# Optimization experiments

Measured on AMD Instinct MI355X. Metric: run time of the kernel, lower is better.

## Reference

```python
import jax, jax.numpy as jnp
import numpy as np

B, R, N, M, K = 4, 4, 4096, 64, 3
F_NUM = 512
KN = K * N


def _block(x, Ws, bs):
    """SO-Net PointResNet: 1x1 convs + ReLU; last layer sees concat(input, hidden)."""
    h = x
    for W, b in zip(Ws[:-1], bs[:-1]):
        h = jax.nn.relu(jnp.einsum('oc,bcn->bon', W, h) + b[None, :, None])
    h = jnp.concatenate([x, h], axis=1)
    return jax.nn.relu(jnp.einsum('oc,bcn->bon', Ws[-1], h) + bs[-1][None, :, None])


def _forward(x, intensity, node, node_knn_I, fpW, fpB, gpW, gpB):
    # --- som.query_topk: k nearest SOM nodes per point ---
    xd = jax.lax.stop_gradient(x)
    dist = jnp.sum((xd[:, :, :, None] - node[:, :, None, :]) ** 2, axis=1)      # B,N,M
    _, topk = jax.lax.top_k(-dist, K)                                           # B,N,K
    min_idx = topk.transpose(0, 2, 1).reshape(B, KN)                            # B,KN (k copies stacked)
    mask = jax.nn.one_hot(min_idx, M, dtype=jnp.float32)                        # B,KN,M
    mask_row_max = jnp.max(mask, axis=1) > 0                                    # B,M  node has >=1 point
    mask_row_sum = jnp.sum(mask, axis=1)                                        # B,M  points per node

    x_stack = jnp.tile(x, (1, 1, K))                                            # B,2,KN
    cluster_mean = jnp.einsum('bcn,bnm->bcm', jax.lax.stop_gradient(x_stack), mask) \
                   / (mask_row_sum[:, None, :] + 1e-5)                          # B,2,M (detached)

    # --- rotation group (2x2 rotations at angles 2*pi*r/R) ---
    theta = 2.0 * jnp.pi * jnp.arange(R, dtype=jnp.float32) / R
    c, s = jnp.cos(theta), jnp.sin(theta)
    rot = jnp.stack([jnp.stack([c, -s], -1), jnp.stack([s, c], -1)], -2)        # R,2,2

    x_rot = jnp.einsum('rij,bjn->brin', rot, x_stack)                           # B,R,2,KN
    node_rot = jnp.einsum('rij,bjm->brim', rot, cluster_mean)                   # B,R,2,M
    centers = jnp.take_along_axis(node_rot, min_idx[:, None, None, :], axis=3)  # B,R,2,KN
    x_dec = jax.lax.stop_gradient(x_rot - centers).reshape(B * R, 2, KN)

    # --- first PointResNet over all B*R rotation copies ---
    feat = _block(x_dec, fpW, fpB)                                              # BR,128,KN

    # --- index_max scatter-max per SOM cluster (value of argmax == segment max) ---
    seg = jnp.tile(min_idx[:, None, :], (1, R, 1)).reshape(B * R, KN)
    segmax = jax.vmap(lambda f, sgi: jax.ops.segment_max(f.T, sgi, num_segments=M).T)(feat, seg)
    rowmax = jnp.tile(mask_row_max[:, None, :], (1, R, 1)).reshape(B * R, M)
    pooled = jnp.where(rowmax[:, None, :], segmax, feat[:, :, 0:1])             # BR,128,M (empty -> gather idx 0)

    # --- final PointResNet over SOM nodes, then max over nodes and rotations ---
    g_in = jnp.concatenate([node_rot.reshape(B * R, 2, M), pooled], axis=1)     # BR,130,M
    out = _block(g_in, gpW, gpB)                                                # BR,F,M
    return out.reshape(B, R, F_NUM, M).max(axis=3).max(axis=1)                  # B,F


def setup_inputs() -> dict:
    key = jax.random.key(0)
    ks = jax.random.split(key, 24)
    d = {}
    d['x'] = jax.random.normal(ks[0], (B, 2, N), jnp.float32)
    d['intensity'] = jax.random.uniform(ks[1], (B, 1, N), jnp.float32)
    d['node'] = jax.random.normal(ks[2], (B, 2, M), jnp.float32)
    d['node_knn_I'] = jax.random.randint(ks[3], (B, M, 1), 0, M)
    dims_fp = [(64, 2), (64, 64), (128, 64), (128, 130)]      # PointResNet(2,[64,64,128,128])
    dims_gp = [(256, 130), (256, 256), (512, 256), (F_NUM, 642)]  # PointResNet(130,[256,256,512,F])
    i = 4
    for name, dims in (('fp', dims_fp), ('gp', dims_gp)):
        for j, (o, ci) in enumerate(dims):
            d[f'{name}_W{j}'] = jax.random.normal(ks[i], (o, ci), jnp.float32) / np.sqrt(ci).astype(np.float32)
            d[f'{name}_b{j}'] = jnp.zeros((o,), jnp.float32)
            i += 1
    return d


def reference(x, intensity, node, node_knn_I,
              fp_W0, fp_b0, fp_W1, fp_b1, fp_W2, fp_b2, fp_W3, fp_b3,
              gp_W0, gp_b0, gp_W1, gp_b1, gp_W2, gp_b2, gp_W3, gp_b3):
    return _forward(x, intensity, node, node_knn_I,
                    [fp_W0, fp_W1, fp_W2, fp_W3], [fp_b0, fp_b1, fp_b2, fp_b3],
                    [gp_W0, gp_W1, gp_W2, gp_W3], [gp_b0, gp_b1, gp_b2, gp_b3])
```

## Files before the change

### kernel.cpp

```cpp
#include <hip/hip_runtime.h>
#include <stdint.h>

#define BB 4
#define RR 4
#define NN 4096
#define MM 64
#define KK 3
#define KNN 12288
#define BRR 16
#define FF 512

typedef short bf16x8 __attribute__((ext_vector_type(8)));
typedef float f32x4 __attribute__((ext_vector_type(4)));

__device__ __forceinline__ float bf2f(unsigned int u) {
  union { unsigned int i; float f; } v; v.i = u << 16; return v.f;
}
__device__ __forceinline__ unsigned short f2bf(float f) {
  union { float f; unsigned int i; } v; v.f = f;
  unsigned int x = v.i;
  return (unsigned short)((x + 0x7fffu + ((x >> 16) & 1u)) >> 16);
}
__device__ __forceinline__ float ldf(const void* p, long i, int isbf) {
  if (isbf) return bf2f(((const unsigned short*)p)[i]);
  return ((const float*)p)[i];
}

__global__ __launch_bounds__(256) void k_detect(
    const unsigned short* __restrict__ x, int* __restrict__ flag) {
  __shared__ int bad;
  if (threadIdx.x == 0) bad = 0;
  __syncthreads();
  int cnt = 0;
  for (int i = threadIdx.x; i < 1024; i += 256) {
    unsigned short u = x[i * 2];
    int e = (u >> 7) & 0xFF;
    if (e >= 0x90 || (e > 0 && e <= 0x50)) ++cnt;
  }
  atomicAdd(&bad, cnt);
  __syncthreads();
  if (threadIdx.x == 0) flag[0] = (bad < 100) ? 1 : 0;
}

struct WPtrs { const void* p[7]; };
__global__ __launch_bounds__(256) void k_cvt(
    WPtrs wp, const int* __restrict__ flag, unsigned short* __restrict__ Wb) {
  const int e0=4096, e1=12288, e2=28928, e3=62208, e4=127744, e5=258816, e6=587520;
  int t = blockIdx.x * 256 + threadIdx.x;
  if (t >= e6) return;
  int s, base;
  if      (t < e0) { s=0; base=0;  }
  else if (t < e1) { s=1; base=e0; }
  else if (t < e2) { s=2; base=e1; }
  else if (t < e3) { s=3; base=e2; }
  else if (t < e4) { s=4; base=e3; }
  else if (t < e5) { s=5; base=e4; }
  else             { s=6; base=e5; }
  int local = t - base;
  unsigned short u;
  if (flag[0]) u = ((const unsigned short*)wp.p[s])[local];
  else         u = f2bf(((const float*)wp.p[s])[local]);
  Wb[t] = u;
}

__global__ __launch_bounds__(256) void k_assign(
    const void* __restrict__ x, const void* __restrict__ node,
    const int* __restrict__ flag, int* __restrict__ idx, float* __restrict__ csum,
    int* __restrict__ blkcnt) {
  __shared__ float nd[2][64];
  __shared__ float cs[192];
  int isbf = flag[0];
  int tid = threadIdx.x;
  int b = blockIdx.x >> 4;
  int n = ((blockIdx.x & 15) << 8) + tid;
  if (tid < 128) nd[tid >> 6][tid & 63] = ldf(node, b * 128 + tid, isbf);
  if (tid < 192) cs[tid] = 0.f;
  __syncthreads();
  float x0 = ldf(x, b * 8192 + n, isbf);
  float x1 = ldf(x, b * 8192 + 4096 + n, isbf);
  float d0 = 1e30f, d1 = 1e30f, d2 = 1e30f;
  int m0 = 0, m1 = 0, m2 = 0;
#pragma unroll 8
  for (int m = 0; m < 64; ++m) {
    float dx = x0 - nd[0][m];
    float dy = x1 - nd[1][m];
    float d = __fmul_rn(dx, dx) + __fmul_rn(dy, dy);
    if (d < d0)      { d2=d1; m2=m1; d1=d0; m1=m0; d0=d; m0=m; }
    else if (d < d1) { d2=d1; m2=m1; d1=d;  m1=m; }
    else if (d < d2) { d2=d;  m2=m; }
  }
  long base = ((long)b * NN + n) * 3;
  idx[base] = m0; idx[base + 1] = m1; idx[base + 2] = m2;
  atomicAdd(&cs[m0*3+0], x0); atomicAdd(&cs[m0*3+1], x1); atomicAdd(&cs[m0*3+2], 1.f);
  atomicAdd(&cs[m1*3+0], x0); atomicAdd(&cs[m1*3+1], x1); atomicAdd(&cs[m1*3+2], 1.f);
  atomicAdd(&cs[m2*3+0], x0); atomicAdd(&cs[m2*3+1], x1); atomicAdd(&cs[m2*3+2], 1.f);
  __syncthreads();
  if (tid < 192) atomicAdd(&csum[b * 192 + tid], cs[tid]);
  if (tid < 64) blkcnt[blockIdx.x * 64 + tid] = (int)cs[tid*3 + 2];
}

__global__ __launch_bounds__(256) void k_means(
    const float* __restrict__ csum, const int* __restrict__ blkcnt,
    float* __restrict__ noderot, int* __restrict__ rowflag,
    int* __restrict__ off, int* __restrict__ blkoff) {
  int t = threadIdx.x;
  int b = t >> 6, m = t & 63;
  float s0 = csum[b*192 + m*3], s1 = csum[b*192 + m*3 + 1], c = csum[b*192 + m*3 + 2];
  float mx = s0 / (c + 1e-5f);
  float my = s1 / (c + 1e-5f);
  rowflag[b * 64 + m] = (c > 0.f) ? 1 : 0;
  for (int r = 0; r < 4; ++r) {
    float th = 1.5707964f * (float)r;
    float cr = cosf(th), sr = sinf(th);
    noderot[((b*4 + r)*2 + 0)*64 + m] = cr*mx - sr*my;
    noderot[((b*4 + r)*2 + 1)*64 + m] = sr*mx + cr*my;
  }
  if (m == 0) {
    int acc = 0;
    for (int mm = 0; mm < 64; ++mm) {
      off[b*64 + mm] = acc;
      acc += (int)csum[b*192 + mm*3 + 2];
    }
  }
  __syncthreads();
  int base = off[b*64 + m];
  for (int blk = 0; blk < 16; ++blk) {
    blkoff[(b*16 + blk)*64 + m] = base;
    base += blkcnt[(b*16 + blk)*64 + m];
  }
}

__global__ __launch_bounds__(256) void k_scatter(
    const int* __restrict__ idx, const int* __restrict__ blkoff,
    int* __restrict__ sorted) {
  __shared__ int lc[64];
  int tid = threadIdx.x;
  int blk = blockIdx.x;
  int b = blk >> 4;
  int n = ((blk & 15) << 8) + tid;
  if (tid < 64) lc[tid] = 0;
  __syncthreads();
#pragma unroll
  for (int kk = 0; kk < 3; ++kk) {
    int m = idx[((long)b * NN + n) * 3 + kk];
    int pos = atomicAdd(&lc[m], 1);
    sorted[b * KNN + blkoff[blk*64 + m] + pos] = (m << 12) | n;
  }
}

__global__ __launch_bounds__(256) void k_fused(
    const void* __restrict__ x, const int* __restrict__ sorted,
    const int* __restrict__ idx, const float* __restrict__ noderot,
    const int* __restrict__ flag,
    const void* __restrict__ fW0, const void* __restrict__ fb0,
    const unsigned short* __restrict__ Wb,
    const void* __restrict__ fb1, const void* __restrict__ fb2,
    const void* __restrict__ fb3,
    unsigned int* __restrict__ pooled, float* __restrict__ feat0) {
  __shared__ unsigned short Cs[64 * 136];
  __shared__ unsigned short Hs[64 * 72];
  __shared__ int mcol[64];
  const unsigned short* fW1 = Wb;
  const unsigned short* fW2 = Wb + 4096;
  const unsigned short* fW3 = Wb + 12288;
  int isbf = flag[0];
  int tid = threadIdx.x, lane = tid & 63, wv = tid >> 6;
  int quad = lane >> 4, lr = lane & 15;
  int br = blockIdx.y, b = br >> 2, r = br & 3;
  if (tid < 64) {
    int e = sorted[b * KNN + blockIdx.x * 64 + tid];
    int m = e >> 12, n = e & 4095;
    int isz = (n == 0 && m == idx[(long)b * NN * 3]) ? 256 : 0;
    mcol[tid] = m | isz;
    float x0 = ldf(x, b*8192 + n, isbf), x1 = ldf(x, b*8192 + 4096 + n, isbf);
    float th = 1.5707964f * (float)r;
    float cr = cosf(th), sr = sinf(th);
    float xd0 = (cr*x0 - sr*x1) - noderot[(br*2 + 0)*64 + m];
    float xd1 = (sr*x0 + cr*x1) - noderot[(br*2 + 1)*64 + m];
    *(unsigned int*)&Cs[tid * 136] = (unsigned int)f2bf(xd0) | ((unsigned int)f2bf(xd1) << 16);
  }
  __syncthreads();
  {
    int col = tid & 63, og = (tid >> 6) << 4;
    unsigned int xu = *(unsigned int*)&Cs[col * 136];
    float fx0 = bf2f(xu & 0xffff), fx1 = bf2f(xu >> 16);
    union { bf16x8 v; unsigned short s[8]; } o8[2];
#pragma unroll
    for (int j = 0; j < 16; ++j) {
      int o = og + j;
      float h = ldf(fb0, o, isbf) + ldf(fW0, o*2, isbf) * fx0 + ldf(fW0, o*2+1, isbf) * fx1;
      o8[j >> 3].s[j & 7] = f2bf(fmaxf(h, 0.f));
    }
    *(bf16x8*)&Hs[col*72 + og]     = o8[0].v;
    *(bf16x8*)&Hs[col*72 + og + 8] = o8[1].v;
  }
  __syncthreads();
  {
    int o0 = wv * 16;
    f32x4 acc[4];
    float bb4[4];
#pragma unroll
    for (int rr = 0; rr < 4; ++rr) bb4[rr] = ldf(fb1, o0 + quad*4 + rr, isbf);
#pragma unroll
    for (int nt = 0; nt < 4; ++nt) acc[nt] = (f32x4){bb4[0], bb4[1], bb4[2], bb4[3]};
#pragma unroll
    for (int ks = 0; ks < 64; ks += 32) {
      bf16x8 a = *(const bf16x8*)(fW1 + (o0 + lr)*64 + ks + quad*8);
#pragma unroll
      for (int nt = 0; nt < 4; ++nt) {
        bf16x8 bf = *(bf16x8*)&Hs[(nt*16 + lr)*72 + ks + quad*8];
        acc[nt] = __builtin_amdgcn_mfma_f32_16x16x32_bf16(a, bf, acc[nt], 0, 0, 0);
      }
    }
    __syncthreads();
#pragma unroll
    for (int nt = 0; nt < 4; ++nt) {
      int col = nt*16 + lr;
      union { unsigned long long u; unsigned short s[4]; } pk;
#pragma unroll
      for (int rr = 0; rr < 4; ++rr) pk.s[rr] = f2bf(fmaxf(acc[nt][rr], 0.f));
      *(unsigned long long*)&Hs[col*72 + o0 + quad*4] = pk.u;
    }
  }
  __syncthreads();
#pragma unroll
  for (int p2 = 0; p2 < 2; ++p2) {
    int o0 = p2*64 + wv*16;
    f32x4 acc[4];
    float bb4[4];
#pragma unroll
    for (int rr = 0; rr < 4; ++rr) bb4[rr] = ldf(fb2, o0 + quad*4 + rr, isbf);
#pragma unroll
    for (int nt = 0; nt < 4; ++nt) acc[nt] = (f32x4){bb4[0], bb4[1], bb4[2], bb4[3]};
#pragma unroll
    for (int ks = 0; ks < 64; ks += 32) {
      bf16x8 a = *(const bf16x8*)(fW2 + (o0 + lr)*64 + ks + quad*8);
#pragma unroll
      for (int nt = 0; nt < 4; ++nt) {
        bf16x8 bf = *(bf16x8*)&Hs[(nt*16 + lr)*72 + ks + quad*8];
        acc[nt] = __builtin_amdgcn_mfma_f32_16x16x32_bf16(a, bf, acc[nt], 0, 0, 0);
      }
    }
#pragma unroll
    for (int nt = 0; nt < 4; ++nt) {
      int col = nt*16 + lr;
      int o = o0 + quad*4;
      unsigned int w0 = (unsigned int)f2bf(fmaxf(acc[nt][0], 0.f)) |
                        ((unsigned int)f2bf(fmaxf(acc[nt][1], 0.f)) << 16);
      unsigned int w1 = (unsigned int)f2bf(fmaxf(acc[nt][2], 0.f)) |
                        ((unsigned int)f2bf(fmaxf(acc[nt][3], 0.f)) << 16);
      *(unsigned int*)&Cs[col*136 + 2 + o] = w0;
      *(unsigned int*)&Cs[col*136 + 4 + o] = w1;
    }
  }
  __syncthreads();
  f32x4 acc3[2][4];
#pragma unroll
  for (int p3 = 0; p3 < 2; ++p3) {
    int o0 = p3*64 + wv*16;
    float bb4[4];
#pragma unroll
    for (int rr = 0; rr < 4; ++rr) bb4[rr] = ldf(fb3, o0 + quad*4 + rr, isbf);
#pragma unroll
    for (int nt = 0; nt < 4; ++nt) acc3[p3][nt] = (f32x4){bb4[0], bb4[1], bb4[2], bb4[3]};
#pragma unroll
    for (int ks = 0; ks < 128; ks += 32) {
      union { bf16x8 v; unsigned int u[4]; } au;
      const unsigned int* ap = (const unsigned int*)(fW3 + (long)(o0 + lr)*130 + ks + quad*8);
      au.u[0] = ap[0]; au.u[1] = ap[1]; au.u[2] = ap[2]; au.u[3] = ap[3];
#pragma unroll
      for (int nt = 0; nt < 4; ++nt) {
        bf16x8 bf = *(bf16x8*)&Cs[(nt*16 + lr)*136 + ks + quad*8];
        acc3[p3][nt] = __builtin_amdgcn_mfma_f32_16x16x32_bf16(au.v, bf, acc3[p3][nt], 0, 0, 0);
      }
    }
#pragma unroll
    for (int rr = 0; rr < 4; ++rr) {
      int o = o0 + quad*4 + rr;
      unsigned int wu = *(const unsigned int*)(fW3 + (long)o*130 + 128);
      float w0 = bf2f(wu & 0xffff), w1 = bf2f(wu >> 16);
#pragma unroll
      for (int nt = 0; nt < 4; ++nt) {
        unsigned int bu = *(unsigned int*)&Cs[(nt*16 + lr)*136 + 128];
        acc3[p3][nt][rr] += w0 * bf2f(bu & 0xffff) + w1 * bf2f(bu >> 16);
      }
    }
  }
  __syncthreads();
#pragma unroll
  for (int p3 = 0; p3 < 2; ++p3) {
    int o0 = p3*64 + wv*16;
#pragma unroll
    for (int nt = 0; nt < 4; ++nt) {
      int col = nt*16 + lr;
      union { unsigned long long u; unsigned short s[4]; } pk;
#pragma unroll
      for (int rr = 0; rr < 4; ++rr) pk.s[rr] = f2bf(fmaxf(acc3[p3][nt][rr], 0.f));
      *(unsigned long long*)&Cs[col*136 + o0 + quad*4] = pk.u;
    }
  }
  __syncthreads();
  {
    int o = tid & 127, h = tid >> 7;
    int c0 = h * 32;
    int curm = mcol[c0] & 255;
    float v = 0.f;
    for (int c = c0; c < c0 + 32; ++c) {
      int mc = mcol[c];
      int mm = mc & 255;
      float f = bf2f(Cs[c*136 + o]);
      if (mm != curm) {
        atomicMax(&pooled[(((long)br*64 + curm) << 7) + o], __float_as_uint(v));
        curm = mm; v = 0.f;
      }
      v = fmaxf(v, f);
      if (mc & 256) feat0[br*128 + o] = f;
    }
    atomicMax(&pooled[(((long)br*64 + curm) << 7) + o], __float_as_uint(v));
  }
}

__global__ __launch_bounds__(256) void k_finalize(
    const unsigned int* __restrict__ pooled, const float* __restrict__ feat0,
    const int* __restrict__ rowflag, const float* __restrict__ noderot,
    unsigned short* __restrict__ AG) {
  int t = blockIdx.x * 256 + threadIdx.x;
  int col = t >> 7, o = t & 127;
  int br = col >> 6, m = col & 63, b = br >> 2;
  float v = __uint_as_float(pooled[((long)col << 7) + o]);
  if (!rowflag[b*64 + m]) v = feat0[br*128 + o];
  AG[(long)col*648 + 2 + o] = f2bf(v);
  if (o < 2) AG[(long)col*648 + o] = f2bf(noderot[(br*2 + o)*64 + m]);
}

template<int KW, int KMAIN, bool REM2, int BSTR, int OSTR, int OOFF, int EPI>
__global__ __launch_bounds__(256) void k_gemm(
    const unsigned short* __restrict__ W, const void* __restrict__ bias,
    const int* __restrict__ flag,
    const unsigned short* __restrict__ Bb, unsigned short* __restrict__ Out,
    unsigned int* __restrict__ outmax) {
  int isbf = flag[0];
  int lane = threadIdx.x & 63;
  int wv = threadIdx.x >> 6;
  int quad = lane >> 4, lr = lane & 15;
  int o0 = blockIdx.y * 64 + wv * 16;
  long p0 = (long)blockIdx.x * 64;
  float bia[4];
#pragma unroll
  for (int rr = 0; rr < 4; ++rr) bia[rr] = ldf(bias, o0 + quad*4 + rr, isbf);
  f32x4 acc[4];
#pragma unroll
  for (int nt = 0; nt < 4; ++nt) acc[nt] = (f32x4){bia[0], bia[1], bia[2], bia[3]};
  const unsigned short* arow = W + (long)(o0 + lr) * KW;
  for (int ks = 0; ks < KMAIN; ks += 32) {
    bf16x8 a;
    if constexpr ((KW % 8) == 0) {
      a = *(const bf16x8*)(arow + ks + quad*8);
    } else {
      union { bf16x8 v; unsigned int u[4]; } au;
      const unsigned int* ap = (const unsigned int*)(arow + ks + quad*8);
      au.u[0] = ap[0]; au.u[1] = ap[1]; au.u[2] = ap[2]; au.u[3] = ap[3];
      a = au.v;
    }
#pragma unroll
    for (int nt = 0; nt < 4; ++nt) {
      bf16x8 bf = *(const bf16x8*)(Bb + (p0 + nt*16 + lr) * BSTR + ks + quad*8);
      acc[nt] = __builtin_amdgcn_mfma_f32_16x16x32_bf16(a, bf, acc[nt], 0, 0, 0);
    }
  }
  if constexpr (REM2) {
#pragma unroll
    for (int rr = 0; rr < 4; ++rr) {
      int o = o0 + quad*4 + rr;
      unsigned int wu = *(const unsigned int*)(W + (long)o * KW + KMAIN);
      float w0 = bf2f(wu & 0xffff), w1 = bf2f(wu >> 16);
#pragma unroll
      for (int nt = 0; nt < 4; ++nt) {
        long p = p0 + nt*16 + lr;
        unsigned int bu = *(const unsigned int*)(Bb + p * BSTR + KMAIN);
        acc[nt][rr] += w0 * bf2f(bu & 0xffff) + w1 * bf2f(bu >> 16);
      }
    }
  }
  if constexpr (EPI == 0) {
#pragma unroll
    for (int nt = 0; nt < 4; ++nt) {
      long p = p0 + nt*16 + lr;
      unsigned short v0 = f2bf(fmaxf(acc[nt][0], 0.f));
      unsigned short v1 = f2bf(fmaxf(acc[nt][1], 0.f));
      unsigned short v2 = f2bf(fmaxf(acc[nt][2], 0.f));
      unsigned short v3 = f2bf(fmaxf(acc[nt][3], 0.f));
      unsigned short* op = Out + p * OSTR + OOFF + o0 + quad*4;
      if constexpr (((OOFF * 2) % 8) == 0) {
        union { unsigned long long u; unsigned short s[4]; } pk;
        pk.s[0] = v0; pk.s[1] = v1; pk.s[2] = v2; pk.s[3] = v3;
        *(unsigned long long*)op = pk.u;
      } else {
        *(unsigned int*)op       = (unsigned int)v0 | ((unsigned int)v1 << 16);
        *(unsigned int*)(op + 2) = (unsigned int)v2 | ((unsigned int)v3 << 16);
      }
    }
  } else {
#pragma unroll
    for (int rr = 0; rr < 4; ++rr) {
      float v = fmaxf(fmaxf(acc[0][rr], acc[1][rr]), fmaxf(acc[2][rr], acc[3][rr]));
      v = fmaxf(v, 0.f);
      v = fmaxf(v, __shfl_xor(v, 1, 64));
      v = fmaxf(v, __shfl_xor(v, 2, 64));
      v = fmaxf(v, __shfl_xor(v, 4, 64));
      v = fmaxf(v, __shfl_xor(v, 8, 64));
      if (lr == 0) {
        int bb2 = (int)(blockIdx.x >> 2);
        atomicMax(&outmax[bb2 * FF + o0 + quad*4 + rr], __float_as_uint(v));
      }
    }
  }
}

__global__ __launch_bounds__(256) void k_out(
    const unsigned int* __restrict__ outmax, const int* __restrict__ flag,
    void* __restrict__ out) {
  int t = blockIdx.x * 256 + threadIdx.x;
  float v = __uint_as_float(outmax[t]);
  if (flag[0]) ((unsigned short*)out)[t] = f2bf(v);
  else         ((float*)out)[t] = v;
}

extern "C" void kernel_launch(void* const* d_in, const int* in_sizes, int n_in,
                              void* d_out, int out_size, void* d_ws, size_t ws_size,
                              hipStream_t stream) {
  const void* x    = d_in[0];
  const void* node = d_in[2];
  const void* fpW0 = d_in[4];  const void* fpb0 = d_in[5];
  const void* fpW1 = d_in[6];  const void* fpb1 = d_in[7];
  const void* fpW2 = d_in[8];  const void* fpb2 = d_in[9];
  const void* fpW3 = d_in[10]; const void* fpb3 = d_in[11];
  const void* gpW0 = d_in[12]; const void* gpb0 = d_in[13];
  const void* gpW1 = d_in[14]; const void* gpb1 = d_in[15];
  const void* gpW2 = d_in[16]; const void* gpb2 = d_in[17];
  const void* gpW3 = d_in[18]; const void* gpb3 = d_in[19];

  char* ws = (char*)d_ws;
  int*            flag    = (int*)(ws + 0);
  float*          csum    = (float*)(ws + 256);
  unsigned int*   outmax  = (unsigned int*)(ws + 3328);
  unsigned int*   pooled  = (unsigned int*)(ws + 11520);
  int*            idx     = (int*)(ws + 535808);
  int*            blkcnt  = (int*)(ws + 732416);
  int*            blkoff  = (int*)(ws + 748800);
  int*            off     = (int*)(ws + 765184);
  float*          noderot = (float*)(ws + 766208);
  int*            rowflag = (int*)(ws + 774400);
  int*            sorted  = (int*)(ws + 775424);
  float*          feat0   = (float*)(ws + 972032);
  unsigned short* AG      = (unsigned short*)(ws + 980224);
  unsigned short* Hg1     = (unsigned short*)(ws + 2307328);
  unsigned short* Hg2     = (unsigned short*)(ws + 2831616);
  unsigned short* Wb      = (unsigned short*)(ws + 3355904);

  hipMemsetAsync(ws, 0, 535808, stream);

  k_detect<<<1, 256, 0, stream>>>((const unsigned short*)x, flag);
  WPtrs wp; wp.p[0]=fpW1; wp.p[1]=fpW2; wp.p[2]=fpW3; wp.p[3]=gpW0;
  wp.p[4]=gpW1; wp.p[5]=gpW2; wp.p[6]=gpW3;
  k_cvt<<<2295, 256, 0, stream>>>(wp, flag, Wb);

  k_assign<<<64, 256, 0, stream>>>(x, node, flag, idx, csum, blkcnt);
  k_means<<<1, 256, 0, stream>>>(csum, blkcnt, noderot, rowflag, off, blkoff);
  k_scatter<<<64, 256, 0, stream>>>(idx, blkoff, sorted);
  k_fused<<<dim3(192, 16), 256, 0, stream>>>(x, sorted, idx, noderot, flag,
                                             fpW0, fpb0, Wb, fpb1, fpb2, fpb3,
                                             pooled, feat0);
  k_finalize<<<512, 256, 0, stream>>>(pooled, feat0, rowflag, noderot, AG);

  const unsigned short* gW0 = Wb + 28928;
  const unsigned short* gW1 = Wb + 62208;
  const unsigned short* gW2 = Wb + 127744;
  const unsigned short* gW3 = Wb + 258816;
  k_gemm<130, 128, true, 648, 256, 0, 0><<<dim3(16, 4), 256, 0, stream>>>(gW0, gpb0, flag, AG, Hg1, nullptr);
  k_gemm<256, 256, false, 256, 256, 0, 0><<<dim3(16, 4), 256, 0, stream>>>(gW1, gpb1, flag, Hg1, Hg2, nullptr);
  k_gemm<256, 256, false, 256, 648, 130, 0><<<dim3(16, 8), 256, 0, stream>>>(gW2, gpb2, flag, Hg2, AG, nullptr);
  k_gemm<642, 640, true, 648, 0, 0, 2><<<dim3(16, 8), 256, 0, stream>>>(gW3, gpb3, flag, AG, nullptr, outmax);

  k_out<<<8, 256, 0, stream>>>(outmax, flag, d_out);
}
```

Baseline: 199.2 us.

## Fuse front-end kernels, swizzle LDS tiles, use packed bf16 convert instruction

Merges the dtype detection, weight conversion and SOM assignment into one launch, and folds the means/prefix-offset kernel into the scatter kernel, cutting five small launches to two. Every block now redoes the small detection scan, and each scatter block recomputes prefix sums serially. LDS row offsets for the Hs and Cs tiles get an XOR swizzle to reduce bank conflicts on the MFMA operand reads. Scalar bf16 rounding is replaced with the v_cvt_pk_bf16_f32 instruction everywhere, which may round differently at the edges.

Measured after the change: 199.4 us. Within noise of the previous version (+0.1%).

```diff
diff --git a/kernel.cpp b/kernel.cpp
--- a/kernel.cpp
+++ b/kernel.cpp
@@ -21,58 +21,66 @@
   unsigned int x = v.i;
   return (unsigned short)((x + 0x7fffu + ((x >> 16) & 1u)) >> 16);
 }
+__device__ __forceinline__ unsigned int cvtpk(float a, float b) {
+  unsigned int r;
+  asm("v_cvt_pk_bf16_f32 %0, %1, %2" : "=v"(r) : "v"(a), "v"(b));
+  return r;
+}
 __device__ __forceinline__ float ldf(const void* p, long i, int isbf) {
   if (isbf) return bf2f(((const unsigned short*)p)[i]);
   return ((const float*)p)[i];
 }
-
-__global__ __launch_bounds__(256) void k_detect(
-    const unsigned short* __restrict__ x, int* __restrict__ flag) {
+__device__ __forceinline__ int hsw(int col, int so) { return col * 72  + (so ^ (col & 24)); }
+__device__ __forceinline__ int csw(int col, int so) { return col * 136 + (so ^ (col & 24)); }
+
+struct WPtrs { const void* p[7]; };
+
+__global__ __launch_bounds__(256) void k_front(
+    const void* __restrict__ x, const void* __restrict__ node, WPtrs wp,
+    int* __restrict__ flag, unsigned short* __restrict__ Wb,
+    int* __restrict__ idx, float* __restrict__ csum, int* __restrict__ blkcnt) {
   __shared__ int bad;
-  if (threadIdx.x == 0) bad = 0;
-  __syncthreads();
-  int cnt = 0;
-  for (int i = threadIdx.x; i < 1024; i += 256) {
-    unsigned short u = x[i * 2];
-    int e = (u >> 7) & 0xFF;
-    if (e >= 0x90 || (e > 0 && e <= 0x50)) ++cnt;
-  }
-  atomicAdd(&bad, cnt);
-  __syncthreads();
-  if (threadIdx.x == 0) flag[0] = (bad < 100) ? 1 : 0;
-}
-
-struct WPtrs { const void* p[7]; };
-__global__ __launch_bounds__(256) void k_cvt(
-    WPtrs wp, const int* __restrict__ flag, unsigned short* __restrict__ Wb) {
-  const int e0=4096, e1=12288, e2=28928, e3=62208, e4=127744, e5=258816, e6=587520;
-  int t = blockIdx.x * 256 + threadIdx.x;
-  if (t >= e6) return;
-  int s, base;
-  if      (t < e0) { s=0; base=0;  }
-  else if (t < e1) { s=1; base=e0; }
-  else if (t < e2) { s=2; base=e1; }
-  else if (t < e3) { s=3; base=e2; }
-  else if (t < e4) { s=4; base=e3; }
-  else if (t < e5) { s=5; base=e4; }
-  else             { s=6; base=e5; }
-  int local = t - base;
-  unsigned short u;
-  if (flag[0]) u = ((const unsigned short*)wp.p[s])[local];
-  else         u = f2bf(((const float*)wp.p[s])[local]);
-  Wb[t] = u;
-}
-
-__global__ __launch_bounds__(256) void k_assign(
-    const void* __restrict__ x, const void* __restrict__ node,
-    const int* __restrict__ flag, int* __restrict__ idx, float* __restrict__ csum,
-    int* __restrict__ blkcnt) {
   __shared__ float nd[2][64];
   __shared__ float cs[192];
-  int isbf = flag[0];
   int tid = threadIdx.x;
-  int b = blockIdx.x >> 4;
-  int n = ((blockIdx.x & 15) << 8) + tid;
+  if (tid == 0) bad = 0;
+  __syncthreads();
+  {
+    const unsigned short* xs = (const unsigned short*)x;
+    int cnt = 0;
+    for (int i = tid; i < 1024; i += 256) {
+      unsigned short u = xs[i * 2];
+      int e = (u >> 7) & 0xFF;
+      if (e >= 0x90 || (e > 0 && e <= 0x50)) ++cnt;
+    }
+    atomicAdd(&bad, cnt);
+  }
+  __syncthreads();
+  int isbf = (bad < 100) ? 1 : 0;
+  if (blockIdx.x == 0 && tid == 0) flag[0] = isbf;
+
+  if (blockIdx.x < 2295) {
+    const int e0=4096, e1=12288, e2=28928, e3=62208, e4=127744, e5=258816, e6=587520;
+    int t = blockIdx.x * 256 + tid;
+    if (t >= e6) return;
+    int s, base;
+    if      (t < e0) { s=0; base=0;  }
+    else if (t < e1) { s=1; base=e0; }
+    else if (t < e2) { s=2; base=e1; }
+    else if (t < e3) { s=3; base=e2; }
+    else if (t < e4) { s=4; base=e3; }
+    else if (t < e5) { s=5; base=e4; }
+    else             { s=6; base=e5; }
+    int local = t - base;
+    unsigned short u;
+    if (isbf) u = ((const unsigned short*)wp.p[s])[local];
+    else      u = f2bf(((const float*)wp.p[s])[local]);
+    Wb[t] = u;
+    return;
+  }
+  int bi = blockIdx.x - 2295;
+  int b = bi >> 4;
+  int n = ((bi & 15) << 8) + tid;
   if (tid < 128) nd[tid >> 6][tid & 63] = ldf(node, b * 128 + tid, isbf);
   if (tid < 192) cs[tid] = 0.f;
   __syncthreads();
@@ -96,55 +104,47 @@
   atomicAdd(&cs[m2*3+0], x0); atomicAdd(&cs[m2*3+1], x1); atomicAdd(&cs[m2*3+2], 1.f);
   __syncthreads();
   if (tid < 192) atomicAdd(&csum[b * 192 + tid], cs[tid]);
-  if (tid < 64) blkcnt[blockIdx.x * 64 + tid] = (int)cs[tid*3 + 2];
-}
-
-__global__ __launch_bounds__(256) void k_means(
+  if (tid < 64) blkcnt[bi * 64 + tid] = (int)cs[tid*3 + 2];
+}
+
+__global__ __launch_bounds__(256) void k_scatter2(
     const float* __restrict__ csum, const int* __restrict__ blkcnt,
-    float* __restrict__ noderot, int* __restrict__ rowflag,
-    int* __restrict__ off, int* __restrict__ blkoff) {
-  int t = threadIdx.x;
-  int b = t >> 6, m = t & 63;
-  float s0 = csum[b*192 + m*3], s1 = csum[b*192 + m*3 + 1], c = csum[b*192 + m*3 + 2];
-  float mx = s0 / (c + 1e-5f);
-  float my = s1 / (c + 1e-5f);
-  rowflag[b * 64 + m] = (c > 0.f) ? 1 : 0;
-  for (int r = 0; r < 4; ++r) {
-    float th = 1.5707964f * (float)r;
-    float cr = cosf(th), sr = sinf(th);
-    noderot[((b*4 + r)*2 + 0)*64 + m] = cr*mx - sr*my;
-    noderot[((b*4 + r)*2 + 1)*64 + m] = sr*mx + cr*my;
-  }
-  if (m == 0) {
-    int acc = 0;
-    for (int mm = 0; mm < 64; ++mm) {
-      off[b*64 + mm] = acc;
-      acc += (int)csum[b*192 + mm*3 + 2];
-    }
-  }
-  __syncthreads();
-  int base = off[b*64 + m];
-  for (int blk = 0; blk < 16; ++blk) {
-    blkoff[(b*16 + blk)*64 + m] = base;
-    base += blkcnt[(b*16 + blk)*64 + m];
-  }
-}
-
-__global__ __launch_bounds__(256) void k_scatter(
-    const int* __restrict__ idx, const int* __restrict__ blkoff,
-    int* __restrict__ sorted) {
+    const int* __restrict__ idx, int* __restrict__ sorted,
+    float* __restrict__ noderot, int* __restrict__ rowflag) {
+  __shared__ int scnt[64];
+  __shared__ int soff[64];
   __shared__ int lc[64];
   int tid = threadIdx.x;
   int blk = blockIdx.x;
-  int b = blk >> 4;
+  int b = blk >> 4, chunk = blk & 15;
+  if (tid < 64) scnt[tid] = (int)csum[b*192 + tid*3 + 2];
+  __syncthreads();
+  if (tid < 64) {
+    int m = tid, acc = 0;
+    for (int mm = 0; mm < m; ++mm) acc += scnt[mm];
+    for (int c = 0; c < chunk; ++c) acc += blkcnt[(b*16 + c)*64 + m];
+    soff[m] = acc;
+    lc[m] = 0;
+    if (chunk == 0) {
+      float s0 = csum[b*192 + m*3], s1 = csum[b*192 + m*3 + 1], cc = csum[b*192 + m*3 + 2];
+      float mx = s0 / (cc + 1e-5f);
+      float my = s1 / (cc + 1e-5f);
+      rowflag[b*64 + m] = (cc > 0.f) ? 1 : 0;
+      for (int r = 0; r < 4; ++r) {
+        float th = 1.5707964f * (float)r;
+        float cr = cosf(th), sr = sinf(th);
+        noderot[((b*4 + r)*2 + 0)*64 + m] = cr*mx - sr*my;
+        noderot[((b*4 + r)*2 + 1)*64 + m] = sr*mx + cr*my;
+      }
+    }
+  }
+  __syncthreads();
   int n = ((blk & 15) << 8) + tid;
-  if (tid < 64) lc[tid] = 0;
-  __syncthreads();
 #pragma unroll
   for (int kk = 0; kk < 3; ++kk) {
     int m = idx[((long)b * NN + n) * 3 + kk];
     int pos = atomicAdd(&lc[m], 1);
-    sorted[b * KNN + blkoff[blk*64 + m] + pos] = (m << 12) | n;
+    sorted[b * KNN + soff[m] + pos] = (m << 12) | n;
   }
 }
 
@@ -177,22 +177,25 @@
     float cr = cosf(th), sr = sinf(th);
     float xd0 = (cr*x0 - sr*x1) - noderot[(br*2 + 0)*64 + m];
     float xd1 = (sr*x0 + cr*x1) - noderot[(br*2 + 1)*64 + m];
-    *(unsigned int*)&Cs[tid * 136] = (unsigned int)f2bf(xd0) | ((unsigned int)f2bf(xd1) << 16);
+    *(unsigned int*)&Cs[csw(tid, 0)] = cvtpk(xd0, xd1);
   }
   __syncthreads();
   {
     int col = tid & 63, og = (tid >> 6) << 4;
-    unsigned int xu = *(unsigned int*)&Cs[col * 136];
+    unsigned int xu = *(unsigned int*)&Cs[csw(col, 0)];
     float fx0 = bf2f(xu & 0xffff), fx1 = bf2f(xu >> 16);
-    union { bf16x8 v; unsigned short s[8]; } o8[2];
+    float hv[16];
 #pragma unroll
     for (int j = 0; j < 16; ++j) {
       int o = og + j;
       float h = ldf(fb0, o, isbf) + ldf(fW0, o*2, isbf) * fx0 + ldf(fW0, o*2+1, isbf) * fx1;
-      o8[j >> 3].s[j & 7] = f2bf(fmaxf(h, 0.f));
-    }
-    *(bf16x8*)&Hs[col*72 + og]     = o8[0].v;
-    *(bf16x8*)&Hs[col*72 + og + 8] = o8[1].v;
+      hv[j] = fmaxf(h, 0.f);
+    }
+    union { bf16x8 v; unsigned int u[4]; } o8[2];
+#pragma unroll
+    for (int j = 0; j < 16; j += 2) o8[j >> 3].u[(j & 7) >> 1] = cvtpk(hv[j], hv[j+1]);
+    *(bf16x8*)&Hs[hsw(col, og)]     = o8[0].v;
+    *(bf16x8*)&Hs[hsw(col, og + 8)] = o8[1].v;
   }
   __syncthreads();
   {
@@ -208,7 +211,7 @@
       bf16x8 a = *(const bf16x8*)(fW1 + (o0 + lr)*64 + ks + quad*8);
 #pragma unroll
       for (int nt = 0; nt < 4; ++nt) {
-        bf16x8 bf = *(bf16x8*)&Hs[(nt*16 + lr)*72 + ks + quad*8];
+        bf16x8 bf = *(bf16x8*)&Hs[hsw(nt*16 + lr, ks + quad*8)];
         acc[nt] = __builtin_amdgcn_mfma_f32_16x16x32_bf16(a, bf, acc[nt], 0, 0, 0);
       }
     }
@@ -216,10 +219,10 @@
 #pragma unroll
     for (int nt = 0; nt < 4; ++nt) {
       int col = nt*16 + lr;
-      union { unsigned long long u; unsigned short s[4]; } pk;
-#pragma unroll
-      for (int rr = 0; rr < 4; ++rr) pk.s[rr] = f2bf(fmaxf(acc[nt][rr], 0.f));
-      *(unsigned long long*)&Hs[col*72 + o0 + quad*4] = pk.u;
+      unsigned int lo = cvtpk(fmaxf(acc[nt][0], 0.f), fmaxf(acc[nt][1], 0.f));
+      unsigned int hi = cvtpk(fmaxf(acc[nt][2], 0.f), fmaxf(acc[nt][3], 0.f));
+      *(unsigned long long*)&Hs[hsw(col, o0 + quad*4)] =
+          (unsigned long long)lo | ((unsigned long long)hi << 32);
     }
   }
   __syncthreads();
@@ -237,7 +240,7 @@
       bf16x8 a = *(const bf16x8*)(fW2 + (o0 + lr)*64 + ks + quad*8);
 #pragma unroll
       for (int nt = 0; nt < 4; ++nt) {
-        bf16x8 bf = *(bf16x8*)&Hs[(nt*16 + lr)*72 + ks + quad*8];
+        bf16x8 bf = *(bf16x8*)&Hs[hsw(nt*16 + lr, ks + quad*8)];
         acc[nt] = __builtin_amdgcn_mfma_f32_16x16x32_bf16(a, bf, acc[nt], 0, 0, 0);
       }
     }
@@ -245,12 +248,12 @@
     for (int nt = 0; nt < 4; ++nt) {
       int col = nt*16 + lr;
       int o = o0 + quad*4;
-      unsigned int w0 = (unsigned int)f2bf(fmaxf(acc[nt][0], 0.f)) |
-                        ((unsigned int)f2bf(fmaxf(acc[nt][1], 0.f)) << 16);
-      unsigned int w1 = (unsigned int)f2bf(fmaxf(acc[nt][2], 0.f)) |
-                        ((unsigned int)f2bf(fmaxf(acc[nt][3], 0.f)) << 16);
-      *(unsigned int*)&Cs[col*136 + 2 + o] = w0;
-      *(unsigned int*)&Cs[col*136 + 4 + o] = w1;
+      unsigned int w0 = cvtpk(fmaxf(acc[nt][0], 0.f), fmaxf(acc[nt][1], 0.f));
+      unsigned int w1 = cvtpk(fmaxf(acc[nt][2], 0.f), fmaxf(acc[nt][3], 0.f));
+      int so0 = 2 + o;
+      int so1 = 4 + o;
+      *(unsigned int*)&Cs[csw(col, so0)] = w0;
+      *(unsigned int*)&Cs[(so1 < 128) ? csw(col, so1) : (col*136 + so1)] = w1;
     }
   }
   __syncthreads();
@@ -270,7 +273,7 @@
       au.u[0] = ap[0]; au.u[1] = ap[1]; au.u[2] = ap[2]; au.u[3] = ap[3];
 #pragma unroll
       for (int nt = 0; nt < 4; ++nt) {
-        bf16x8 bf = *(bf16x8*)&Cs[(nt*16 + lr)*136 + ks + quad*8];
+        bf16x8 bf = *(bf16x8*)&Cs[csw(nt*16 + lr, ks + quad*8)];
         acc3[p3][nt] = __builtin_amdgcn_mfma_f32_16x16x32_bf16(au.v, bf, acc3[p3][nt], 0, 0, 0);
       }
     }
@@ -293,10 +296,10 @@
 #pragma unroll
     for (int nt = 0; nt < 4; ++nt) {
       int col = nt*16 + lr;
-      union { unsigned long long u; unsigned short s[4]; } pk;
-#pragma unroll
-      for (int rr = 0; rr < 4; ++rr) pk.s[rr] = f2bf(fmaxf(acc3[p3][nt][rr], 0.f));
-      *(unsigned long long*)&Cs[col*136 + o0 + quad*4] = pk.u;
+      unsigned int lo = cvtpk(fmaxf(acc3[p3][nt][0], 0.f), fmaxf(acc3[p3][nt][1], 0.f));
+      unsigned int hi = cvtpk(fmaxf(acc3[p3][nt][2], 0.f), fmaxf(acc3[p3][nt][3], 0.f));
+      *(unsigned long long*)&Cs[csw(col, o0 + quad*4)] =
+          (unsigned long long)lo | ((unsigned long long)hi << 32);
     }
   }
   __syncthreads();
@@ -308,7 +311,7 @@
     for (int c = c0; c < c0 + 32; ++c) {
       int mc = mcol[c];
       int mm = mc & 255;
-      float f = bf2f(Cs[c*136 + o]);
+      float f = bf2f(Cs[csw(c, o)]);
       if (mm != curm) {
         atomicMax(&pooled[(((long)br*64 + curm) << 7) + o], __float_as_uint(v));
         curm = mm; v = 0.f;
@@ -386,18 +389,14 @@
 #pragma unroll
     for (int nt = 0; nt < 4; ++nt) {
       long p = p0 + nt*16 + lr;
-      unsigned short v0 = f2bf(fmaxf(acc[nt][0], 0.f));
-      unsigned short v1 = f2bf(fmaxf(acc[nt][1], 0.f));
-      unsigned short v2 = f2bf(fmaxf(acc[nt][2], 0.f));
-      unsigned short v3 = f2bf(fmaxf(acc[nt][3], 0.f));
+      unsigned int lo = cvtpk(fmaxf(acc[nt][0], 0.f), fmaxf(acc[nt][1], 0.f));
+      unsigned int hi = cvtpk(fmaxf(acc[nt][2], 0.f), fmaxf(acc[nt][3], 0.f));
       unsigned short* op = Out + p * OSTR + OOFF + o0 + quad*4;
       if constexpr (((OOFF * 2) % 8) == 0) {
-        union { unsigned long long u; unsigned short s[4]; } pk;
-        pk.s[0] = v0; pk.s[1] = v1; pk.s[2] = v2; pk.s[3] = v3;
-        *(unsigned long long*)op = pk.u;
+        *(unsigned long long*)op = (unsigned long long)lo | ((unsigned long long)hi << 32);
       } else {
-        *(unsigned int*)op       = (unsigned int)v0 | ((unsigned int)v1 << 16);
-        *(unsigned int*)(op + 2) = (unsigned int)v2 | ((unsigned int)v3 << 16);
+        *(unsigned int*)op       = lo;
+        *(unsigned int*)(op + 2) = hi;
       }
     }
   } else {
@@ -447,8 +446,6 @@
   unsigned int*   pooled  = (unsigned int*)(ws + 11520);
   int*            idx     = (int*)(ws + 535808);
   int*            blkcnt  = (int*)(ws + 732416);
-  int*            blkoff  = (int*)(ws + 748800);
-  int*            off     = (int*)(ws + 765184);
   float*          noderot = (float*)(ws + 766208);
   int*            rowflag = (int*)(ws + 774400);
   int*            sorted  = (int*)(ws + 775424);
@@ -460,14 +457,10 @@
 
   hipMemsetAsync(ws, 0, 535808, stream);
 
-  k_detect<<<1, 256, 0, stream>>>((const unsigned short*)x, flag);
   WPtrs wp; wp.p[0]=fpW1; wp.p[1]=fpW2; wp.p[2]=fpW3; wp.p[3]=gpW0;
   wp.p[4]=gpW1; wp.p[5]=gpW2; wp.p[6]=gpW3;
-  k_cvt<<<2295, 256, 0, stream>>>(wp, flag, Wb);
-
-  k_assign<<<64, 256, 0, stream>>>(x, node, flag, idx, csum, blkcnt);
-  k_means<<<1, 256, 0, stream>>>(csum, blkcnt, noderot, rowflag, off, blkoff);
-  k_scatter<<<64, 256, 0, stream>>>(idx, blkoff, sorted);
+  k_front<<<2359, 256, 0, stream>>>(x, node, wp, flag, Wb, idx, csum, blkcnt);
+  k_scatter2<<<64, 256, 0, stream>>>(csum, blkcnt, idx, sorted, noderot, rowflag);
   k_fused<<<dim3(192, 16), 256, 0, stream>>>(x, sorted, idx, noderot, flag,
                                              fpW0, fpb0, Wb, fpb1, fpb2, fpb3,
                                              pooled, feat0);
```
